# Optimization experiments

Measured on AMD Instinct MI355X. Metric: run time of the kernel, lower is better.

The kernel has to match this reference:

```python
import jax, jax.numpy as jnp
import numpy as np

D_MODEL = 1024
D_OUT = 1024
N_EXPERTS = 8
TOP_K = 2


def setup_inputs() -> dict:
    key = jax.random.key(0)
    ks = jax.random.split(key, 5)
    b, t = 4, 4096
    inputs = jax.random.normal(ks[0], (b, t, D_MODEL), dtype=jnp.float32)
    # gate: Linear(input_dim, num_experts) -> weight (E, d), bias (E,)
    Wg = jax.random.normal(ks[1], (N_EXPERTS, D_MODEL), dtype=jnp.float32) / np.sqrt(D_MODEL)
    bg = jnp.zeros((N_EXPERTS,), dtype=jnp.float32)
    # experts: E x Linear(input_dim, output_dim) -> (E, d, f) and (E, f)
    We = jax.random.normal(ks[2], (N_EXPERTS, D_MODEL, D_OUT), dtype=jnp.float32) / np.sqrt(D_MODEL)
    be = jnp.zeros((N_EXPERTS, D_OUT), dtype=jnp.float32)
    return {"inputs": inputs, "Wg": Wg, "bg": bg, "We": We, "be": be}


def reference(inputs, Wg, bg, We, be):
    # gate logits: (b, t, E)
    gate_logits = jnp.einsum('btd,ed->bte', inputs, Wg) + bg
    # top-k per token (values descending, distinct indices) -> (b, t, k)
    topv, topi = jax.lax.top_k(gate_logits, TOP_K)
    gatew = jax.nn.sigmoid(topv).astype(inputs.dtype)            # (b, t, k)
    # scatter the k gate weights into a dense per-expert combine weight (b, t, E)
    onehot = jax.nn.one_hot(topi, N_EXPERTS, dtype=inputs.dtype)  # (b, t, k, E)
    combine = jnp.einsum('btk,btke->bte', gatew, onehot)          # (b, t, E)
    # per-expert linear outputs for all tokens: (b, t, E, f)
    expert_out = jnp.einsum('btd,edf->btef', inputs, We) + be
    # weighted combine over experts (unselected experts have weight 0)
    results = jnp.einsum('bte,btef->btf', combine, expert_out)
    return results
```

## Files before the change

kernel.cpp:

```cpp
#include <hip/hip_runtime.h>
#include <math.h>

#define DM 1024
#define DF 1024
#define NE 8
#define NBIN 16
#define MAXT 136
#define BM 128
#define BN 64
#define BKT 32
#define NT 32

typedef __bf16 bf16x8 __attribute__((ext_vector_type(8)));
typedef __bf16 bf16x4 __attribute__((ext_vector_type(4)));
typedef float floatx4 __attribute__((ext_vector_type(4)));

typedef const __attribute__((address_space(1))) unsigned int* gas_t;
typedef __attribute__((address_space(3))) unsigned int* las_t;

__device__ __forceinline__ void ld_lds16(const void* g, void* l) {
    __builtin_amdgcn_global_load_lds((gas_t)g, (las_t)l, 16, 0, 0);
}

#define WAITVM(N) asm volatile("s_waitcnt vmcnt(" #N ")" ::: "memory")
#define BARRIER() do { asm volatile("" ::: "memory"); \
                       __builtin_amdgcn_s_barrier(); \
                       asm volatile("" ::: "memory"); } while (0)


__global__ void convert_weT(const float* __restrict__ We, __bf16* __restrict__ WeT) {
    int n  = blockIdx.x * 256 + threadIdx.x;
    int kc = blockIdx.y * 8;
    int e  = blockIdx.z;
    const float* src = We + ((size_t)e << 20) + (size_t)kc * DF + n;
    bf16x8 v;
#pragma unroll
    for (int j = 0; j < 8; ++j) v[j] = (__bf16)src[(size_t)j * DF];
    *(bf16x8*)&WeT[((size_t)e << 20) + (size_t)n * DM + kc] = v;
}

__global__ void gate_kernel(const float4* __restrict__ X4, const float4* __restrict__ Wg4,
                            const float* __restrict__ bg, int* __restrict__ tok_e,
                            float* __restrict__ tok_w, __bf16* __restrict__ Xb, int T) {
    int wid  = threadIdx.x >> 6;
    int lane = threadIdx.x & 63;
    int t = blockIdx.x * 4 + wid;
    if (t >= T) return;
    float acc[NE] = {};
    float4 xs[4];
#pragma unroll
    for (int c = 0; c < 4; ++c) {
        float4 xv = X4[(size_t)t * 256 + c * 64 + lane];
        xs[c] = xv;
#pragma unroll
        for (int e = 0; e < NE; ++e) {
            float4 wv = Wg4[e * 256 + c * 64 + lane];
            acc[e] += xv.x * wv.x + xv.y * wv.y + xv.z * wv.z + xv.w * wv.w;
        }
    }
#pragma unroll
    for (int c = 0; c < 4; ++c) {
        bf16x4 v;
        v[0] = (__bf16)xs[c].x; v[1] = (__bf16)xs[c].y;
        v[2] = (__bf16)xs[c].z; v[3] = (__bf16)xs[c].w;
        *(bf16x4*)&Xb[(size_t)t * DM + c * 256 + lane * 4] = v;
    }
#pragma unroll
    for (int e = 0; e < NE; ++e) {
#pragma unroll
        for (int off = 32; off > 0; off >>= 1)
            acc[e] += __shfl_down(acc[e], off, 64);
    }
    if (lane == 0) {
        float l[NE];
#pragma unroll
        for (int e = 0; e < NE; ++e) l[e] = acc[e] + bg[e];
        int b0 = 0; float v0 = l[0];
        for (int e = 1; e < NE; ++e) if (l[e] > v0) { v0 = l[e]; b0 = e; }
        int b1 = -1; float v1 = -3.4e38f;
        for (int e = 0; e < NE; ++e) if (e != b0 && l[e] > v1) { v1 = l[e]; b1 = e; }
        tok_e[2 * t]     = b0;  tok_e[2 * t + 1] = b1;
        tok_w[2 * t]     = 1.f / (1.f + expf(-v0));
        tok_w[2 * t + 1] = 1.f / (1.f + expf(-v1));
    }
}

__global__ void hist_kernel(const int* __restrict__ tok_e, int* __restrict__ blk_cnt, int n) {
    int b = blockIdx.x, tid = threadIdx.x;
    int idx  = b * 256 + tid;
    int lane = tid & 63, w = tid >> 6;
    int bin = (idx < n) ? ((idx & 1) * NE + tok_e[idx]) : -1;
    __shared__ int wc[4][NBIN];
#pragma unroll
    for (int bx = 0; bx < NBIN; ++bx) {
        unsigned long long m = __ballot(bin == bx);
        if (lane == 0) wc[w][bx] = (int)__popcll(m);
    }
    __syncthreads();
    if (tid < NBIN) blk_cnt[b * NBIN + tid] = wc[0][tid] + wc[1][tid] + wc[2][tid] + wc[3][tid];
}

__global__ void scan_kernel(const int* __restrict__ blk_cnt, int* __restrict__ blk_base,
                            int4* __restrict__ wl, int* __restrict__ ntiles, int NB) {
    __shared__ int c[2048];
    __shared__ int tot[NBIN], base[NBIN];
    int tid = threadIdx.x;
    for (int i = tid; i < NB * NBIN; i += 256) c[i] = blk_cnt[i];
    __syncthreads();
    if (tid < NBIN) {
        int s = 0;
        for (int b = 0; b < NB; ++b) s += c[b * NBIN + tid];
        tot[tid] = s;
    }
    __syncthreads();
    if (tid == 0) {
        int s = 0;
        for (int b = 0; b < NBIN; ++b) { base[b] = s; s += tot[b]; }
    }
    __syncthreads();
    if (tid < NBIN) {
        int run = base[tid];
        for (int b = 0; b < NB; ++b) { int v = c[b * NBIN + tid]; c[b * NBIN + tid] = run; run += v; }
    }
    __syncthreads();
    for (int i = tid; i < NB * NBIN; i += 256) blk_base[i] = c[i];
    if (tid == 0) {
        for (int p = 0; p < 2; ++p) {
            int nt = 0;
            for (int e = 0; e < NE; ++e) {
                int bin = p * NE + e;
                int cnt = tot[bin], sg = base[bin];
                for (int r0 = 0; r0 < cnt; r0 += BM)
                    wl[p * MAXT + nt++] = make_int4(e, r0, sg, cnt);
            }
            ntiles[p] = nt;
        }
    }
}

__global__ void scatter_kernel(const int* __restrict__ tok_e, const float* __restrict__ tok_w,
                               const int* __restrict__ blk_base, int* __restrict__ gath_tok,
                               float* __restrict__ gath_w, int n) {
    int b = blockIdx.x, tid = threadIdx.x;
    int idx  = b * 256 + tid;
    int lane = tid & 63, w = tid >> 6;
    bool act = idx < n;
    int bin = act ? ((idx & 1) * NE + tok_e[idx]) : -1;
    __shared__ int wc[4][NBIN], wb[4][NBIN];
    int myrank = 0;
#pragma unroll
    for (int bx = 0; bx < NBIN; ++bx) {
        unsigned long long m = __ballot(bin == bx);
        if (lane == 0) wc[w][bx] = (int)__popcll(m);
        if (bin == bx) myrank = (int)__popcll(m & ((1ull << lane) - 1ull));
    }
    __syncthreads();
    if (tid < NBIN) {
        int run = blk_base[b * NBIN + tid];
#pragma unroll
        for (int wv = 0; wv < 4; ++wv) { wb[wv][tid] = run; run += wc[wv][tid]; }
    }
    __syncthreads();
    if (act) {
        int pos = wb[w][bin] + myrank;
        gath_tok[pos] = idx >> 1;
        gath_w[pos]   = tok_w[idx];
    }
}

template <bool ACC>
__global__ __launch_bounds__(256) void expert_gemm_mfma(
        const __bf16* __restrict__ Xb, const __bf16* __restrict__ WeT,
        const float* __restrict__ be, const int4* __restrict__ wl,
        const int* __restrict__ ntiles, const int* __restrict__ gtok,
        const float* __restrict__ gw, float* __restrict__ out) {
    int sw = (blockIdx.x & 7) * (2 * MAXT) + (blockIdx.x >> 3);
    int tix  = sw >> 4;
    int col0 = (sw & 15) * BN;
    if (tix >= ntiles[0]) return;
    int4 ent = wl[tix];
    int e = ent.x, row0 = ent.y, seg = ent.z, n_e = ent.w;

    __shared__ __align__(16) char smem[49152];
    __bf16* Asb = (__bf16*)smem;
    __bf16* Bsb = (__bf16*)(smem + 32768);
    float*  Cs  = (float*)smem;
    __shared__ int   s_tok[BM];
    __shared__ float s_w[BM];

    int tid = threadIdx.x;
    if (tid < BM) {
        int gr = row0 + tid;
        s_tok[tid] = (gr < n_e) ? gtok[seg + gr] : gtok[seg];
        s_w[tid]   = (gr < n_e) ? gw[seg + gr]   : 0.f;
    }
    __syncthreads();

    int lane = tid & 63, w = tid >> 6;
    int rsub = lane >> 2;
    int kc   = (lane & 3) ^ ((lane >> 3) & 3);

    const __bf16* aptr0 = Xb + (size_t)s_tok[w * 16 + rsub] * DM + kc * 8;
    const __bf16* aptr1 = Xb + (size_t)s_tok[(4 + w) * 16 + rsub] * DM + kc * 8;
    const __bf16* bptr  = WeT + ((size_t)e << 20)
                        + (size_t)(col0 + w * 16 + rsub) * DM + kc * 8;

    int wr  = (w >> 1) * 64;
    int wcc = (w & 1) * 32;
    int m16 = lane & 15, q4 = lane >> 4;
    int ccu = q4 ^ ((m16 >> 1) & 3);

    floatx4 acc[4][2] = {};

#define STAGE(B, KS) do { \
    ld_lds16(aptr0 + (KS) * BKT, Asb + (B) * 4096 + w * 512); \
    ld_lds16(aptr1 + (KS) * BKT, Asb + (B) * 4096 + (4 + w) * 512); \
    ld_lds16(bptr  + (KS) * BKT, Bsb + (B) * 2048 + w * 512); } while (0)

#define COMP(B) do { \
    bf16x8 af[4], bfr[2]; \
    _Pragma("unroll") \
    for (int i = 0; i < 4; ++i) \
        af[i] = *(const bf16x8*)&Asb[(B) * 4096 + (wr + i * 16 + m16) * 32 + ccu * 8]; \
    _Pragma("unroll") \
    for (int j = 0; j < 2; ++j) \
        bfr[j] = *(const bf16x8*)&Bsb[(B) * 2048 + (wcc + j * 16 + m16) * 32 + ccu * 8]; \
    _Pragma("unroll") \
    for (int i = 0; i < 4; ++i) \
        _Pragma("unroll") \
        for (int j = 0; j < 2; ++j) \
            acc[i][j] = __builtin_amdgcn_mfma_f32_16x16x32_bf16(af[i], bfr[j], acc[i][j], 0, 0, 0); \
    } while (0)

    STAGE(0, 0); STAGE(1, 1); STAGE(2, 2);
    WAITVM(6);
    BARRIER();

    for (int kk = 0; kk < NT - 4; kk += 4) {
        COMP(0); BARRIER(); STAGE(3, kk + 3); WAITVM(6); BARRIER();
        COMP(1); BARRIER(); STAGE(0, kk + 4); WAITVM(6); BARRIER();
        COMP(2); BARRIER(); STAGE(1, kk + 5); WAITVM(6); BARRIER();
        COMP(3); BARRIER(); STAGE(2, kk + 6); WAITVM(6); BARRIER();
    }
    COMP(0); BARRIER(); STAGE(3, NT - 1); WAITVM(6); BARRIER();
    COMP(1); BARRIER(); WAITVM(3); BARRIER();
    COMP(2); BARRIER(); WAITVM(0); BARRIER();
    COMP(3); BARRIER();

#undef STAGE
#undef COMP

#pragma unroll
    for (int j = 0; j < 2; ++j) {
#pragma unroll
        for (int i = 0; i < 4; ++i) {
#pragma unroll
            for (int rg = 0; rg < 4; ++rg) {
                int rl = wr + i * 16 + q4 * 4 + rg;
                int cl = wcc + j * 16 + m16;
                int cq = (cl >> 2) ^ (rl & 15);
                Cs[rl * 64 + cq * 4 + (cl & 3)] = acc[i][j][rg];
            }
        }
    }
    BARRIER();

#pragma unroll
    for (int rh = 0; rh < 2; ++rh) {
        int rr = w * 32 + rh * 16 + (lane >> 2);
        int gr2 = row0 + rr;
        if (gr2 < n_e) {
            int tok = s_tok[rr];
            float wgt = s_w[rr];
            float* orow = out + (size_t)tok * DF + col0;
            const float* brow = be + e * DF + col0;
#pragma unroll
            for (int kq = 0; kq < 4; ++kq) {
                int cq_log = kq * 4 + (lane & 3);
                int c4 = cq_log * 4;
                floatx4 v  = *(const floatx4*)&Cs[rr * 64 + ((cq_log ^ (rr & 15)) * 4)];
                floatx4 bv = *(const floatx4*)&brow[c4];
                floatx4 r;
#pragma unroll
                for (int z = 0; z < 4; ++z) r[z] = wgt * (v[z] + bv[z]);
                if (ACC) {
                    floatx4 o = *(const floatx4*)&orow[c4];
#pragma unroll
                    for (int z = 0; z < 4; ++z) r[z] += o[z];
                }
                *(floatx4*)&orow[c4] = r;
            }
        }
    }
}

extern "C" void kernel_launch(void* const* d_in, const int* in_sizes, int n_in,
                              void* d_out, int out_size, void* d_ws, size_t ws_size,
                              hipStream_t stream) {
    const float* x  = (const float*)d_in[0];
    const float* Wg = (const float*)d_in[1];
    const float* bg = (const float*)d_in[2];
    const float* We = (const float*)d_in[3];
    const float* be = (const float*)d_in[4];
    float* out = (float*)d_out;

    int T = in_sizes[0] / DM;
    int n_slots = 2 * T;
    int NB = (n_slots + 255) / 256;

    char* ws = (char*)d_ws;
    size_t xb_bytes  = (size_t)T * DM * 2;
    size_t weT_bytes = (size_t)NE * DM * DF * 2;
    __bf16* Xb  = (__bf16*)ws;
    __bf16* WeT = (__bf16*)(ws + xb_bytes);
    char* rt = ws + xb_bytes + weT_bytes;
    int*   ntiles    = (int*)(rt + 0);
    int4*  wl        = (int4*)(rt + 64);
    int*   blk_cnt   = (int*)(rt + 64 + 2 * MAXT * 16);
    int*   blk_base  = (int*)((char*)blk_cnt + (size_t)NB * NBIN * 4);
    int*   tok_e     = (int*)((char*)blk_base + (size_t)NB * NBIN * 4);
    float* tok_w     = (float*)((char*)tok_e + (size_t)n_slots * 4);
    int*   gath_tok  = (int*)((char*)tok_w + (size_t)n_slots * 4);
    float* gath_w    = (float*)((char*)gath_tok + (size_t)n_slots * 4);

    convert_weT<<<dim3(DF / 256, DM / 8, NE), 256, 0, stream>>>(We, WeT);
    gate_kernel<<<(T + 3) / 4, 256, 0, stream>>>((const float4*)x, (const float4*)Wg,
                                                 bg, tok_e, tok_w, Xb, T);
    hist_kernel<<<NB, 256, 0, stream>>>(tok_e, blk_cnt, n_slots);
    scan_kernel<<<1, 256, 0, stream>>>(blk_cnt, blk_base, wl, ntiles, NB);
    scatter_kernel<<<NB, 256, 0, stream>>>(tok_e, tok_w, blk_base, gath_tok, gath_w, n_slots);

    expert_gemm_mfma<false><<<MAXT * 16, 256, 0, stream>>>(Xb, WeT, be, wl, ntiles,
                                                           gath_tok, gath_w, out);
    expert_gemm_mfma<true><<<MAXT * 16, 256, 0, stream>>>(Xb, WeT, be, wl + MAXT, ntiles + 1,
                                                          gath_tok, gath_w, out);
}
```

Before: 310.9 us.

## Fuse preprocessing kernels and shrink expert GEMM pipeline to three stages

Merges the weight transpose-convert and gate kernels into one launch that dispatches on block index. It also folds the histogram and scan into a single 1024-thread block that uses LDS atomics, removing two launches and the intermediate count buffer. The expert GEMM drops from a 4-deep to a 3-deep LDS ring, cutting shared memory so more blocks can fit per CU, at the cost of less load-latency hiding. The single-block histogram now walks all slots serially, which adds work on one CU.

Result: slower. 338.0 us (+8.7%).

```diff
diff --git a/kernel.cpp b/kernel.cpp
--- a/kernel.cpp
+++ b/kernel.cpp
@@ -28,23 +28,26 @@
                        asm volatile("" ::: "memory"); } while (0)
 
 
-__global__ void convert_weT(const float* __restrict__ We, __bf16* __restrict__ WeT) {
-    int n  = blockIdx.x * 256 + threadIdx.x;
-    int kc = blockIdx.y * 8;
-    int e  = blockIdx.z;
-    const float* src = We + ((size_t)e << 20) + (size_t)kc * DF + n;
-    bf16x8 v;
-#pragma unroll
-    for (int j = 0; j < 8; ++j) v[j] = (__bf16)src[(size_t)j * DF];
-    *(bf16x8*)&WeT[((size_t)e << 20) + (size_t)n * DM + kc] = v;
-}
-
-__global__ void gate_kernel(const float4* __restrict__ X4, const float4* __restrict__ Wg4,
-                            const float* __restrict__ bg, int* __restrict__ tok_e,
-                            float* __restrict__ tok_w, __bf16* __restrict__ Xb, int T) {
-    int wid  = threadIdx.x >> 6;
-    int lane = threadIdx.x & 63;
-    int t = blockIdx.x * 4 + wid;
+__global__ void fused_pre(const float* __restrict__ We, __bf16* __restrict__ WeT,
+                          const float4* __restrict__ X4, const float4* __restrict__ Wg4,
+                          const float* __restrict__ bg, int* __restrict__ tok_e,
+                          float* __restrict__ tok_w, __bf16* __restrict__ Xb, int T) {
+    int bid = blockIdx.x;
+    int tid = threadIdx.x;
+    if (bid < 4096) {
+        int bz = bid >> 9, rem = bid & 511, by = rem >> 2, bx = rem & 3;
+        int n  = bx * 256 + tid;
+        int kc = by * 8;
+        const float* src = We + ((size_t)bz << 20) + (size_t)kc * DF + n;
+        bf16x8 v;
+#pragma unroll
+        for (int j = 0; j < 8; ++j) v[j] = (__bf16)src[(size_t)j * DF];
+        *(bf16x8*)&WeT[((size_t)bz << 20) + (size_t)n * DM + kc] = v;
+        return;
+    }
+    int wid  = tid >> 6;
+    int lane = tid & 63;
+    int t = (bid - 4096) * 4 + wid;
     if (t >= T) return;
     float acc[NE] = {};
     float4 xs[4];
@@ -85,31 +88,29 @@
     }
 }
 
-__global__ void hist_kernel(const int* __restrict__ tok_e, int* __restrict__ blk_cnt, int n) {
-    int b = blockIdx.x, tid = threadIdx.x;
-    int idx  = b * 256 + tid;
-    int lane = tid & 63, w = tid >> 6;
-    int bin = (idx < n) ? ((idx & 1) * NE + tok_e[idx]) : -1;
-    __shared__ int wc[4][NBIN];
-#pragma unroll
-    for (int bx = 0; bx < NBIN; ++bx) {
-        unsigned long long m = __ballot(bin == bx);
-        if (lane == 0) wc[w][bx] = (int)__popcll(m);
-    }
-    __syncthreads();
-    if (tid < NBIN) blk_cnt[b * NBIN + tid] = wc[0][tid] + wc[1][tid] + wc[2][tid] + wc[3][tid];
-}
-
-__global__ void scan_kernel(const int* __restrict__ blk_cnt, int* __restrict__ blk_base,
-                            int4* __restrict__ wl, int* __restrict__ ntiles, int NB) {
-    __shared__ int c[2048];
+__global__ void hist_scan(const int* __restrict__ tok_e, int* __restrict__ blk_base,
+                          int4* __restrict__ wl, int* __restrict__ ntiles,
+                          int n, int NB) {
+    __shared__ int cnt[2048];
     __shared__ int tot[NBIN], base[NBIN];
     int tid = threadIdx.x;
-    for (int i = tid; i < NB * NBIN; i += 256) c[i] = blk_cnt[i];
+    int lane = tid & 63, w = tid >> 6;
+    for (int i = tid; i < NB * NBIN; i += 1024) cnt[i] = 0;
+    __syncthreads();
+    for (int b0 = 0; b0 < n; b0 += 1024) {
+        int idx = b0 + tid;
+        int bin = (idx < n) ? ((idx & 1) * NE + tok_e[idx]) : -1;
+        int seg = (b0 >> 8) + (w >> 2);
+#pragma unroll
+        for (int bx = 0; bx < NBIN; ++bx) {
+            unsigned long long m = __ballot(bin == bx);
+            if (lane == 0 && m) atomicAdd(&cnt[seg * NBIN + bx], (int)__popcll(m));
+        }
+    }
     __syncthreads();
     if (tid < NBIN) {
         int s = 0;
-        for (int b = 0; b < NB; ++b) s += c[b * NBIN + tid];
+        for (int b = 0; b < NB; ++b) s += cnt[b * NBIN + tid];
         tot[tid] = s;
     }
     __syncthreads();
@@ -120,18 +121,20 @@
     __syncthreads();
     if (tid < NBIN) {
         int run = base[tid];
-        for (int b = 0; b < NB; ++b) { int v = c[b * NBIN + tid]; c[b * NBIN + tid] = run; run += v; }
-    }
-    __syncthreads();
-    for (int i = tid; i < NB * NBIN; i += 256) blk_base[i] = c[i];
+        for (int b = 0; b < NB; ++b) {
+            int v = cnt[b * NBIN + tid];
+            blk_base[b * NBIN + tid] = run;
+            run += v;
+        }
+    }
     if (tid == 0) {
         for (int p = 0; p < 2; ++p) {
             int nt = 0;
             for (int e = 0; e < NE; ++e) {
                 int bin = p * NE + e;
-                int cnt = tot[bin], sg = base[bin];
-                for (int r0 = 0; r0 < cnt; r0 += BM)
-                    wl[p * MAXT + nt++] = make_int4(e, r0, sg, cnt);
+                int c = tot[bin], sg = base[bin];
+                for (int r0 = 0; r0 < c; r0 += BM)
+                    wl[p * MAXT + nt++] = make_int4(e, r0, sg, c);
             }
             ntiles[p] = nt;
         }
@@ -181,9 +184,9 @@
     int4 ent = wl[tix];
     int e = ent.x, row0 = ent.y, seg = ent.z, n_e = ent.w;
 
-    __shared__ __align__(16) char smem[49152];
+    __shared__ __align__(16) char smem[36864];
     __bf16* Asb = (__bf16*)smem;
-    __bf16* Bsb = (__bf16*)(smem + 32768);
+    __bf16* Bsb = (__bf16*)(smem + 24576);
     float*  Cs  = (float*)smem;
     __shared__ int   s_tok[BM];
     __shared__ float s_w[BM];
@@ -232,20 +235,18 @@
             acc[i][j] = __builtin_amdgcn_mfma_f32_16x16x32_bf16(af[i], bfr[j], acc[i][j], 0, 0, 0); \
     } while (0)
 
-    STAGE(0, 0); STAGE(1, 1); STAGE(2, 2);
-    WAITVM(6);
+    STAGE(0, 0); STAGE(1, 1);
+    WAITVM(3);
     BARRIER();
 
-    for (int kk = 0; kk < NT - 4; kk += 4) {
-        COMP(0); BARRIER(); STAGE(3, kk + 3); WAITVM(6); BARRIER();
-        COMP(1); BARRIER(); STAGE(0, kk + 4); WAITVM(6); BARRIER();
-        COMP(2); BARRIER(); STAGE(1, kk + 5); WAITVM(6); BARRIER();
-        COMP(3); BARRIER(); STAGE(2, kk + 6); WAITVM(6); BARRIER();
-    }
-    COMP(0); BARRIER(); STAGE(3, NT - 1); WAITVM(6); BARRIER();
-    COMP(1); BARRIER(); WAITVM(3); BARRIER();
-    COMP(2); BARRIER(); WAITVM(0); BARRIER();
-    COMP(3); BARRIER();
+    for (int kk = 0; kk < NT - 2; kk += 3) {
+        COMP(0); BARRIER(); STAGE(2, kk + 2); WAITVM(3); BARRIER();
+        COMP(1); BARRIER(); STAGE(0, kk + 3); WAITVM(3); BARRIER();
+        COMP(2); BARRIER(); STAGE(1, kk + 4); WAITVM(3); BARRIER();
+    }
+    COMP(0); WAITVM(0); BARRIER();
+    COMP(1);
+    BARRIER();
 
 #undef STAGE
 #undef COMP
@@ -323,11 +324,11 @@
     int*   gath_tok  = (int*)((char*)tok_w + (size_t)n_slots * 4);
     float* gath_w    = (float*)((char*)gath_tok + (size_t)n_slots * 4);
 
-    convert_weT<<<dim3(DF / 256, DM / 8, NE), 256, 0, stream>>>(We, WeT);
-    gate_kernel<<<(T + 3) / 4, 256, 0, stream>>>((const float4*)x, (const float4*)Wg,
-                                                 bg, tok_e, tok_w, Xb, T);
-    hist_kernel<<<NB, 256, 0, stream>>>(tok_e, blk_cnt, n_slots);
-    scan_kernel<<<1, 256, 0, stream>>>(blk_cnt, blk_base, wl, ntiles, NB);
+    int gate_blocks = (T + 3) / 4;
+    fused_pre<<<4096 + gate_blocks, 256, 0, stream>>>(We, WeT, (const float4*)x,
+                                                      (const float4*)Wg, bg,
+                                                      tok_e, tok_w, Xb, T);
+    hist_scan<<<1, 1024, 0, stream>>>(tok_e, blk_base, wl, ntiles, n_slots, NB);
     scatter_kernel<<<NB, 256, 0, stream>>>(tok_e, tok_w, blk_base, gath_tok, gath_w, n_slots);
 
     expert_gemm_mfma<false><<<MAXT * 16, 256, 0, stream>>>(Xb, WeT, be, wl, ntiles,
```
